# Kernel optimization log

Hardware: AMD Instinct MI355X
Metric: run time of the kernel (lower is better)

The kernel has to match this reference:

```python
import jax, jax.numpy as jnp
import numpy as np

N_NODES = 2048
UNITS = 64
IN_DIM = 64
K_DIFF = 2  # max_diffusion_step


def _rw_norm_t(adj):
    # random-walk normalize D^{-1}(A+I), then transpose (as in forward())
    a = adj + jnp.eye(adj.shape[0], dtype=adj.dtype)
    d = jnp.sum(a, axis=1)
    d_inv = jnp.where(d > 0, 1.0 / jnp.where(d > 0, d, 1.0), 0.0)
    return (d_inv[:, None] * a).T


def _gconv(x_cat, adj_t, W, b):
    # x_cat: (B, N, F). Chebyshev-like diffusion: x0, A x0, 2 A x1 - x0, ...
    x0 = x_cat
    xs = [x0]
    x1 = jnp.einsum('nm,bmf->bnf', adj_t, x0)
    xs.append(x1)
    for _ in range(2, K_DIFF + 1):
        x2 = 2.0 * jnp.einsum('nm,bmf->bnf', adj_t, x1) - x0
        xs.append(x2)
        x0, x1 = x1, x2
    x = jnp.stack(xs, axis=-1)  # (B, N, F, K+1) -> matches torch permute(3,1,2,0)
    B, N, F, K = x.shape
    x = x.reshape(B * N, F * K)
    out = x @ W + b
    return out.reshape(B, N, -1)


def setup_inputs() -> dict:
    key = jax.random.key(0)
    ks = jax.random.split(key, 6)
    B = 64
    inputs = jax.random.normal(ks[0], (B, N_NODES * IN_DIM), dtype=jnp.float32)
    hx = jax.random.normal(ks[1], (B, N_NODES * UNITS), dtype=jnp.float32)
    adj = jax.random.uniform(ks[2], (N_NODES, N_NODES), dtype=jnp.float32)
    in_sz = IN_DIM + UNITS
    nm = K_DIFF + 1
    scale = float(np.sqrt(2.0 / (in_sz * nm + 2 * UNITS)))  # xavier-ish
    W_ru = jax.random.normal(ks[3], (in_sz * nm, 2 * UNITS), dtype=jnp.float32) * scale
    b_ru = jnp.ones((2 * UNITS,), dtype=jnp.float32)  # bias_start=1.0
    W_c = jax.random.normal(ks[4], (in_sz * nm, UNITS), dtype=jnp.float32) * scale
    b_c = jnp.zeros((UNITS,), dtype=jnp.float32)
    return {"inputs": inputs, "hx": hx, "adj": adj,
            "W_ru": W_ru, "b_ru": b_ru, "W_c": W_c, "b_c": b_c}


def reference(inputs, hx, adj, W_ru, b_ru, W_c, b_c):
    B = inputs.shape[0]
    x = inputs.reshape(B, N_NODES, IN_DIM)
    h = hx.reshape(B, N_NODES, UNITS)
    adj_t = _rw_norm_t(adj)
    # r/u gates via graph conv + sigmoid
    ru = jax.nn.sigmoid(_gconv(jnp.concatenate([x, h], axis=-1), adj_t, W_ru, b_ru))
    r, u = ru[..., :UNITS], ru[..., UNITS:]
    # candidate state
    c = jnp.tanh(_gconv(jnp.concatenate([x, r * h], axis=-1), adj_t, W_c, b_c))
    new_state = u * h + (1.0 - u) * c
    return new_state.reshape(B, N_NODES * UNITS)
```

## Files before the change

kernel.cpp:

```cpp
#include <hip/hip_runtime.h>
#include <math.h>

typedef __attribute__((ext_vector_type(8))) short short8;
typedef __attribute__((ext_vector_type(4))) float float4v;
typedef __attribute__((ext_vector_type(16))) float float16v;
typedef __attribute__((ext_vector_type(4))) unsigned short ushort4v;
typedef unsigned short u16;
typedef unsigned int u32;

#define NB 64
#define NN 2048
#define FD 128
#define UD 64
#define KT 384


__device__ __forceinline__ u16 f2bf(float f) {
    unsigned int u = __float_as_uint(f);
    u += 0x7fffu + ((u >> 16) & 1u);
    return (u16)(u >> 16);
}
__device__ __forceinline__ float bf2f(u16 s) {
    return __uint_as_float(((unsigned int)s) << 16);
}
__device__ __forceinline__ float sigmoidf_(float x) {
    return 1.0f / (1.0f + expf(-x));
}
__device__ __forceinline__ void gl2lds16(const u16* g, u16* l) {
    __builtin_amdgcn_global_load_lds((const __attribute__((address_space(1))) unsigned int*)g,
                                     (__attribute__((address_space(3))) unsigned int*)l,
                                     16, 0, 0);
}

__global__ void k_rownorm(const float* __restrict__ adj, float* __restrict__ d_inv) {
    int m = blockIdx.x;
    const float4v* row = (const float4v*)(adj + (size_t)m * NN);
    float s = 0.f;
    for (int i = threadIdx.x; i < NN / 4; i += 256) {
        float4v v = row[i];
        s += v.x + v.y + v.z + v.w;
    }
    __shared__ float red[4];
    for (int off = 32; off; off >>= 1) s += __shfl_down(s, off, 64);
    if ((threadIdx.x & 63) == 0) red[threadIdx.x >> 6] = s;
    __syncthreads();
    if (threadIdx.x == 0) {
        float t = red[0] + red[1] + red[2] + red[3] + 1.0f;
        d_inv[m] = 1.0f / t;
    }
}

__global__ void k_adjT(const float* __restrict__ adj, const float* __restrict__ d_inv,
                       u16* __restrict__ adjT) {
    __shared__ u16 T[64 * 72];
    int m0 = blockIdx.x * 64;
    int n0 = blockIdx.y * 64;
    int t = threadIdx.x;
    for (int p = 0; p < 4; ++p) {
        int idx = t + 256 * p;
        int i  = idx >> 4;
        int n4 = idx & 15;
        int m = m0 + i;
        float4v v = *(const float4v*)(adj + (size_t)m * NN + n0 + n4 * 4);
        float di = d_inv[m];
        float vv[4] = {v.x, v.y, v.z, v.w};
#pragma unroll
        for (int j = 0; j < 4; ++j) {
            int n = n0 + n4 * 4 + j;
            float a = vv[j] + ((m == n) ? 1.0f : 0.0f);
            T[(n4 * 4 + j) * 72 + i] = f2bf(a * di);
        }
    }
    __syncthreads();
#pragma unroll
    for (int p = 0; p < 2; ++p) {
        int S = t + 256 * p;
        int rgl = S >> 8, kgl = (S >> 7) & 1, s = S & 127;
        int c = s >> 5, r = s & 31;
        short8 v = *(const short8*)(T + (rgl * 32 + r) * 72 + kgl * 32 + c * 8);
        *(short8*)(adjT + ((size_t)((n0 >> 5) + rgl) * 64 + (m0 >> 5) + kgl) * 1024 + s * 8) = v;
    }
}

__global__ void k_reorderW(const float* __restrict__ W, u16* __restrict__ Wt, int OD) {
    int idx = blockIdx.x * 256 + threadIdx.x;
    if (idx >= KT * OD) return;
    int o  = idx % OD;
    int kp = idx / OD;
    int kd = kp >> 7, f = kp & 127;
    Wt[(size_t)o * KT + kp] = f2bf(W[(size_t)(f * 3 + kd) * OD + o]);
}

__global__ void k_xcat(const float* __restrict__ x, const float* __restrict__ h,
                       u16* __restrict__ X0c) {
    __shared__ u16 T[128 * 136];
    int m0 = blockIdx.x * 128;
    int b  = blockIdx.y;
    int t = threadIdx.x;
    const float* srcs[2] = { x + (size_t)b * (NN * 64), h + (size_t)b * (NN * 64) };
    for (int s = 0; s < 2; ++s) {
        const float* src = srcs[s];
        for (int p = 0; p < 8; ++p) {
            int idx = t + 256 * p;
            int mi = idx >> 4;
            int f4 = idx & 15;
            float4v v = *(const float4v*)(src + (size_t)(m0 + mi) * 64 + f4 * 4);
            float vv[4] = {v.x, v.y, v.z, v.w};
#pragma unroll
            for (int j = 0; j < 4; ++j)
                T[(s * 64 + f4 * 4 + j) * 136 + mi] = f2bf(vv[j]);
        }
    }
    __syncthreads();
#pragma unroll
    for (int p = 0; p < 8; ++p) {
        int S = t + 256 * p;
        int fgl = S >> 9, kgl = (S >> 7) & 3, s = S & 127;
        int c = s >> 5, r = s & 31;
        short8 v = *(const short8*)(T + (fgl * 32 + r) * 136 + kgl * 32 + c * 8);
        *(short8*)(X0c + ((size_t)(b * 4 + fgl) * 64 + (m0 >> 5) + kgl) * 1024 + s * 8) = v;
    }
}

template<int MT>
__global__ __launch_bounds__(256, 2)
void k_gemm(const u16* __restrict__ A, const u16* __restrict__ Bc,
            u16* __restrict__ Cc, const u16* __restrict__ Sub, int mode, int cBlocks) {
    __shared__ u16 SM[8192 + 4096 * MT];
    u16* A0 = SM;            u16* A1 = SM + 4096;
    u16* B0 = SM + 8192;     u16* B1 = SM + 8192 + 2048 * MT;

    int id = blockIdx.x + cBlocks * blockIdx.y;
    int band = cBlocks >> 3;
    int g = id & 7, s = id >> 3;
    int cb = g * band + (s % band);
    int nb = s / band;
    int c0 = cb * (64 * MT);
    int n0 = nb * 128;

    int t = threadIdx.x;
    int wave = t >> 6, lane = t & 63;
    int wy = wave & 1, wx = wave >> 1;
    int ln = lane & 31, hi = lane >> 5;
    int l16 = lane * 8;

    const u16* gaP[2];
#pragma unroll
    for (int i = 0; i < 2; ++i) {
        int T = t + 256 * i;
        gaP[i] = A + ((size_t)((n0 >> 5) + (T >> 7)) * 64) * 1024 + (size_t)(T & 127) * 8;
    }
    const u16* gbP[MT];
#pragma unroll
    for (int i = 0; i < MT; ++i) {
        int T = t + 256 * i;
        gbP[i] = Bc + ((size_t)((c0 >> 5) + (T >> 7)) * 64) * 1024 + (size_t)(T & 127) * 8;
    }

    float16v acc[MT][2];
#pragma unroll
    for (int i = 0; i < MT; ++i)
#pragma unroll
        for (int j = 0; j < 2; ++j)
#pragma unroll
            for (int e = 0; e < 16; ++e) acc[i][j][e] = 0.f;

#pragma unroll
    for (int i = 0; i < 2; ++i)  gl2lds16(gaP[i], A0 + (t + 256 * i) * 8);
#pragma unroll
    for (int i = 0; i < MT; ++i) gl2lds16(gbP[i], B0 + (t + 256 * i) * 8);

#pragma unroll 2
    for (int it = 0; it < 64; ++it) {
        u16* Ac = (it & 1) ? A1 : A0;
        u16* Bs = (it & 1) ? B1 : B0;
        __syncthreads();
        if (it + 1 < 64) {
            int ko = (it + 1) * 1024;
            u16* An = (it & 1) ? A0 : A1;
            u16* Bn = (it & 1) ? B0 : B1;
#pragma unroll
            for (int i = 0; i < 2; ++i)  gl2lds16(gaP[i] + ko, An + (t + 256 * i) * 8);
#pragma unroll
            for (int i = 0; i < MT; ++i) gl2lds16(gbP[i] + ko, Bn + (t + 256 * i) * 8);
        }
        short8 fa[2][MT], fb[2][2];
#pragma unroll
        for (int ks = 0; ks < 2; ++ks) {
#pragma unroll
            for (int mt = 0; mt < MT; ++mt)
                fa[ks][mt] = *(const short8*)(Bs + ((wx * MT + mt) * 2 + ks) * 512 + l16);
#pragma unroll
            for (int nt = 0; nt < 2; ++nt)
                fb[ks][nt] = *(const short8*)(Ac + ((wy * 2 + nt) * 2 + ks) * 512 + l16);
        }
#pragma unroll
        for (int ks = 0; ks < 2; ++ks)
#pragma unroll
            for (int mt = 0; mt < MT; ++mt)
#pragma unroll
                for (int nt = 0; nt < 2; ++nt)
                    acc[mt][nt] = __builtin_amdgcn_mfma_f32_32x32x16_bf16(fa[ks][mt], fb[ks][nt], acc[mt][nt], 0, 0, 0);
    }

    __syncthreads();
#pragma unroll
    for (int p = 0; p < 2; ++p) {
        if (p) __syncthreads();
        if (wx == p) {
#pragma unroll
            for (int mt = 0; mt < MT; ++mt)
#pragma unroll
                for (int nt = 0; nt < 2; ++nt)
#pragma unroll
                    for (int e = 0; e < 16; ++e) {
                        int cl = mt * 32 + 4 * hi + 8 * (e >> 2) + (e & 3);
                        int nl = wy * 64 + nt * 32 + ln;
                        SM[cl * 136 + nl] = f2bf(acc[mt][nt][e]);
                    }
        }
        __syncthreads();
#pragma unroll
        for (int pp = 0; pp < 2 * MT; ++pp) {
            int S = t + 256 * pp;
            int rgl = S >> 9, kgl = (S >> 7) & 3, sl = S & 127;
            int c = sl >> 5, r = sl & 31;
            short8 v = *(const short8*)(SM + (rgl * 32 + r) * 136 + kgl * 32 + c * 8);
            size_t gaddr = ((size_t)((c0 >> 5) + p * MT + rgl) * 64 + (n0 >> 5) + kgl) * 1024 + sl * 8;
            if (mode == 1) {
                short8 sv = *(const short8*)(Sub + gaddr);
                short8 o;
#pragma unroll
                for (int e = 0; e < 8; ++e)
                    o[e] = (short)f2bf(2.f * bf2f((u16)v[e]) - bf2f((u16)sv[e]));
                *(short8*)(Cc + gaddr) = o;
            } else {
                *(short8*)(Cc + gaddr) = v;
            }
        }
    }
}

__global__ __launch_bounds__(256)
void k_ruW(const u16* __restrict__ X0c, const u16* __restrict__ X1c, const u16* __restrict__ X2c,
           const u16* __restrict__ Wt, const float* __restrict__ bias,
           const float* __restrict__ hx,
           u16* __restrict__ RH0c, float* __restrict__ Utc) {
    __shared__ u16 As[128 * 40];
    __shared__ u16 Bs[4096];
    int rt = blockIdx.x;
    int b  = rt >> 4;
    int m0 = (rt & 15) * 128;
    int t = threadIdx.x;
    int wave = t >> 6, lane = t & 63;
    int wr = (wave >> 1) * 64, wc = (wave & 1) * 64;
    int lr = lane & 15, q = lane >> 4;
    const u16* Xs[3] = {X0c, X1c, X2c};
    int f2 = t & 15;
    int m8 = (t >> 4) * 8;
    const u16* gw[2];
#pragma unroll
    for (int i = 0; i < 2; ++i) {
        int T = t + 256 * i;
        gw[i] = Wt + (size_t)((T >> 6) * 16 + (T & 15)) * KT + ((T >> 4) & 3) * 8;
    }

    float4v acc[4][4];
#pragma unroll
    for (int i = 0; i < 4; ++i)
#pragma unroll
        for (int j = 0; j < 4; ++j) { acc[i][j].x = 0.f; acc[i][j].y = 0.f; acc[i][j].z = 0.f; acc[i][j].w = 0.f; }

    for (int it = 0; it < 12; ++it) {
        int k0 = it * 32;
        int kd = k0 >> 7, fb = k0 & 127;
        gl2lds16(gw[0] + k0, Bs + t * 8);
        gl2lds16(gw[1] + k0, Bs + (t + 256) * 8);
        const u16* base = Xs[kd] + ((size_t)(b * 4 + (fb >> 5)) * 64 + (m0 >> 5) + (m8 >> 5)) * 1024
                          + (((m8 >> 3) & 3) * 32 + 2 * f2) * 8;
        short8 v0 = *(const short8*)(base);
        short8 v1 = *(const short8*)(base + 8);
#pragma unroll
        for (int e = 0; e < 8; ++e)
            *(u32*)(As + (m8 + e) * 40 + 2 * f2) = (u32)(u16)v0[e] | ((u32)(u16)v1[e] << 16);
        __syncthreads();
        short8 af[4], bfr[4];
#pragma unroll
        for (int i = 0; i < 4; ++i) af[i]  = *(const short8*)(As + (wr + 16 * i + lr) * 40 + q * 8);
#pragma unroll
        for (int j = 0; j < 4; ++j) bfr[j] = *(const short8*)(Bs + ((wc >> 4) + j) * 512 + lane * 8);
#pragma unroll
        for (int i = 0; i < 4; ++i)
#pragma unroll
            for (int j = 0; j < 4; ++j)
                acc[i][j] = __builtin_amdgcn_mfma_f32_16x16x32_bf16(af[i], bfr[j], acc[i][j], 0, 0, 0);
        __syncthreads();
    }
#pragma unroll
    for (int i = 0; i < 4; ++i) {
        int m = m0 + wr + 16 * i + q * 4;
#pragma unroll
        for (int j = 0; j < 4; ++j) {
            int o = wc + 16 * j + lr;
            float bia = bias[o];
            float4v v = acc[i][j];
            if (o < 64) {
                ushort4v pk;
#pragma unroll
                for (int r = 0; r < 4; ++r) {
                    float sg = sigmoidf_(v[r] + bia);
                    float hh = hx[(size_t)b * (NN * 64) + (size_t)(m + r) * 64 + o];
                    pk[r] = f2bf(sg * hh);
                }
                size_t ga = ((size_t)(b * 2 + (o >> 5)) * 64 + (m >> 5)) * 1024
                            + (((m >> 3) & 3) * 32 + (o & 31)) * 8 + (m & 7);
                *(ushort4v*)(RH0c + ga) = pk;
            } else {
                int gg = o - 64;
                float4v u;
#pragma unroll
                for (int r = 0; r < 4; ++r) u[r] = sigmoidf_(v[r] + bia);
                *(float4v*)(Utc + ((size_t)(b * UD + gg)) * NN + m) = u;
            }
        }
    }
}

__global__ __launch_bounds__(256)
void k_cW(const u16* __restrict__ X0c, const u16* __restrict__ X1c, const u16* __restrict__ X2c,
          const u16* __restrict__ RH0c, const u16* __restrict__ RH1c, const u16* __restrict__ RH2c,
          const u16* __restrict__ Wt, const float* __restrict__ bias,
          const float* __restrict__ hx, const float* __restrict__ Utc,
          float* __restrict__ out) {
    __shared__ u16 As[256 * 40];
    __shared__ u16 Bs[2048];
    int rt = blockIdx.x;
    int b  = rt >> 3;
    int m0 = (rt & 7) * 256;
    int t = threadIdx.x;
    int wave = t >> 6, lane = t & 63;
    int lr = lane & 15, q = lane >> 4;
    const u16* Xs[3] = {X0c, X1c, X2c};
    const u16* Rs[3] = {RH0c, RH1c, RH2c};
    const u16* gw = Wt + (size_t)((t >> 6) * 16 + (t & 15)) * KT + ((t >> 4) & 3) * 8;

    float4v acc[4][4];
#pragma unroll
    for (int i = 0; i < 4; ++i)
#pragma unroll
        for (int j = 0; j < 4; ++j) { acc[i][j].x = 0.f; acc[i][j].y = 0.f; acc[i][j].z = 0.f; acc[i][j].w = 0.f; }

    for (int it = 0; it < 12; ++it) {
        int k0 = it * 32;
        int kd = k0 >> 7, fb = k0 & 127;
        const u16* mat; int rg;
        if (fb < 64) { mat = Xs[kd]; rg = b * 4 + (fb >> 5); }
        else         { mat = Rs[kd]; rg = b * 2 + ((fb - 64) >> 5); }
        gl2lds16(gw + k0, Bs + t * 8);
#pragma unroll
        for (int p = 0; p < 2; ++p) {
            int idx = t + 256 * p;
            int f2 = idx & 15;
            int m8 = (idx >> 4) * 8;
            const u16* base = mat + ((size_t)rg * 64 + (m0 >> 5) + (m8 >> 5)) * 1024
                              + (((m8 >> 3) & 3) * 32 + 2 * f2) * 8;
            short8 v0 = *(const short8*)(base);
            short8 v1 = *(const short8*)(base + 8);
#pragma unroll
            for (int e = 0; e < 8; ++e)
                *(u32*)(As + (m8 + e) * 40 + 2 * f2) = (u32)(u16)v0[e] | ((u32)(u16)v1[e] << 16);
        }
        __syncthreads();
        short8 af[4], bfr[4];
#pragma unroll
        for (int i = 0; i < 4; ++i) af[i]  = *(const short8*)(As + (64 * wave + 16 * i + lr) * 40 + q * 8);
#pragma unroll
        for (int j = 0; j < 4; ++j) bfr[j] = *(const short8*)(Bs + j * 512 + lane * 8);
#pragma unroll
        for (int i = 0; i < 4; ++i)
#pragma unroll
            for (int j = 0; j < 4; ++j)
                acc[i][j] = __builtin_amdgcn_mfma_f32_16x16x32_bf16(af[i], bfr[j], acc[i][j], 0, 0, 0);
        __syncthreads();
    }
#pragma unroll
    for (int i = 0; i < 4; ++i) {
        int m = m0 + 64 * wave + 16 * i + q * 4;
#pragma unroll
        for (int j = 0; j < 4; ++j) {
            int o = 16 * j + lr;
            float bia = bias[o];
            float4v v = acc[i][j];
            float4v u = *(const float4v*)(Utc + ((size_t)(b * UD + o)) * NN + m);
#pragma unroll
            for (int r = 0; r < 4; ++r) {
                float c = tanhf(v[r] + bia);
                size_t idx = (size_t)b * (NN * 64) + (size_t)(m + r) * 64 + o;
                float hh = hx[idx];
                out[idx] = u[r] * hh + (1.0f - u[r]) * c;
            }
        }
    }
}

extern "C" void kernel_launch(void* const* d_in, const int* in_sizes, int n_in,
                              void* d_out, int out_size, void* d_ws, size_t ws_size,
                              hipStream_t stream) {
    const float* x    = (const float*)d_in[0];
    const float* hx   = (const float*)d_in[1];
    const float* adj  = (const float*)d_in[2];
    const float* W_ru = (const float*)d_in[3];
    const float* b_ru = (const float*)d_in[4];
    const float* W_c  = (const float*)d_in[5];
    const float* b_c  = (const float*)d_in[6];
    float* out = (float*)d_out;

    char* ws = (char*)d_ws;
    size_t off = 0;
    auto alloc = [&](size_t bytes) -> void* {
        void* p = ws + off;
        off += (bytes + 255) & ~(size_t)255;
        return p;
    };
    float* d_inv = (float*)alloc((size_t)NN * 4);
    u16* adjT  = (u16*)alloc((size_t)NN * NN * 2);
    u16* Wt_ru = (u16*)alloc((size_t)FD * KT * 2);
    u16* Wt_c  = (u16*)alloc((size_t)UD * KT * 2);
    u16* X0c = (u16*)alloc((size_t)NB * FD * NN * 2);
    u16* X1c = (u16*)alloc((size_t)NB * FD * NN * 2);
    u16* X2c = (u16*)alloc((size_t)NB * FD * NN * 2);
    u16* RH0c = (u16*)alloc((size_t)NB * UD * NN * 2);
    u16* RH1c = (u16*)alloc((size_t)NB * UD * NN * 2);
    u16* RH2c = (u16*)alloc((size_t)NB * UD * NN * 2);
    float* Utc = (float*)alloc((size_t)NB * UD * NN * 4);

    k_rownorm<<<dim3(NN), dim3(256), 0, stream>>>(adj, d_inv);
    k_adjT<<<dim3(32, 32), dim3(256), 0, stream>>>(adj, d_inv, adjT);
    k_reorderW<<<dim3((KT * FD + 255) / 256), dim3(256), 0, stream>>>(W_ru, Wt_ru, FD);
    k_reorderW<<<dim3((KT * UD + 255) / 256), dim3(256), 0, stream>>>(W_c, Wt_c, UD);
    k_xcat<<<dim3(16, NB), dim3(256), 0, stream>>>(x, hx, X0c);
    k_gemm<4><<<dim3(32, 16), dim3(256), 0, stream>>>(adjT, X0c, X1c, X0c, 0, 32);
    k_gemm<4><<<dim3(32, 16), dim3(256), 0, stream>>>(adjT, X1c, X2c, X0c, 1, 32);
    k_ruW<<<dim3(1024), dim3(256), 0, stream>>>(X0c, X1c, X2c, Wt_ru, b_ru, hx, RH0c, Utc);
    k_gemm<2><<<dim3(32, 16), dim3(256), 0, stream>>>(adjT, RH0c, RH1c, RH0c, 0, 32);
    k_gemm<2><<<dim3(32, 16), dim3(256), 0, stream>>>(adjT, RH1c, RH2c, RH0c, 1, 32);
    k_cW<<<dim3(512), dim3(256), 0, stream>>>(X0c, X1c, X2c, RH0c, RH1c, RH2c, Wt_c, b_c, hx, Utc, out);
}
```

Measured before the change: 472.0 us.

## Emit MFMA-fragment layout from diffusion GEMMs and rewrite projection kernels

The diffusion GEMMs now write their results straight from accumulators into a second MFMA-fragment-ordered layout, and they only do the LDS transpose into the feature-major layout when the next diffusion step needs it. The projection kernels are rewritten to stream both operands into double-buffered LDS with 32x32 MFMA and no per-element repacking. The update gate is stored as bf16 in node-major order rather than fp32 transposed. Together these aim to remove the register-level reshuffle in the projections, cut redundant transposes and gate traffic, and overlap loads with compute. The cost is an extra full-size buffer write in the first diffusion step and some extra workspace.

```diff
diff --git a/kernel.cpp b/kernel.cpp
--- a/kernel.cpp
+++ b/kernel.cpp
@@ -88,11 +88,12 @@
     int o  = idx % OD;
     int kp = idx / OD;
     int kd = kp >> 7, f = kp & 127;
-    Wt[(size_t)o * KT + kp] = f2bf(W[(size_t)(f * 3 + kd) * OD + o]);
+    size_t dst = ((size_t)(o >> 5) * 12 + (kp >> 5)) * 1024 + (((kp >> 3) & 3) * 32 + (o & 31)) * 8 + (kp & 7);
+    Wt[dst] = f2bf(W[(size_t)(f * 3 + kd) * OD + o]);
 }
 
 __global__ void k_xcat(const float* __restrict__ x, const float* __restrict__ h,
-                       u16* __restrict__ X0c) {
+                       u16* __restrict__ X0f, u16* __restrict__ X0m) {
     __shared__ u16 T[128 * 136];
     int m0 = blockIdx.x * 128;
     int b  = blockIdx.y;
@@ -118,14 +119,27 @@
         int fgl = S >> 9, kgl = (S >> 7) & 3, s = S & 127;
         int c = s >> 5, r = s & 31;
         short8 v = *(const short8*)(T + (fgl * 32 + r) * 136 + kgl * 32 + c * 8);
-        *(short8*)(X0c + ((size_t)(b * 4 + fgl) * 64 + (m0 >> 5) + kgl) * 1024 + s * 8) = v;
+        *(short8*)(X0f + ((size_t)(b * 4 + fgl) * 64 + (m0 >> 5) + kgl) * 1024 + s * 8) = v;
+    }
+#pragma unroll
+    for (int p = 0; p < 8; ++p) {
+        int S = t + 256 * p;
+        int fc = S >> 7;
+        int mi = S & 127;
+        short8 v;
+#pragma unroll
+        for (int e = 0; e < 8; ++e) v[e] = (short)T[(fc * 8 + e) * 136 + mi];
+        size_t dst = ((size_t)(b * 64 + (m0 >> 5) + (mi >> 5)) * 4 + (fc >> 2)) * 1024
+                     + ((fc & 3) * 32 + (mi & 31)) * 8;
+        *(short8*)(X0m + dst) = v;
     }
 }
 
 template<int MT>
 __global__ __launch_bounds__(256, 2)
 void k_gemm(const u16* __restrict__ A, const u16* __restrict__ Bc,
-            u16* __restrict__ Cc, const u16* __restrict__ Sub, int mode, int cBlocks) {
+            u16* __restrict__ outF, u16* __restrict__ outM,
+            const u16* __restrict__ Sub, int mode, int cBlocks) {
     __shared__ u16 SM[8192 + 4096 * MT];
     u16* A0 = SM;            u16* A1 = SM + 4096;
     u16* B0 = SM + 8192;     u16* B1 = SM + 8192 + 2048 * MT;
@@ -203,204 +217,249 @@
                     acc[mt][nt] = __builtin_amdgcn_mfma_f32_32x32x16_bf16(fa[ks][mt], fb[ks][nt], acc[mt][nt], 0, 0, 0);
     }
 
+    int bb2 = 2 * cb + wx;
+#pragma unroll
+    for (int mt = 0; mt < MT; ++mt) {
+#pragma unroll
+        for (int nt = 0; nt < 2; ++nt) {
+            int mg = (n0 >> 5) + wy * 2 + nt;
+            size_t pbase = ((size_t)(bb2 * 64 + mg) * MT + mt) * 1024;
+#pragma unroll
+            for (int eq = 0; eq < 4; ++eq) {
+                size_t addr = pbase + (eq * 32 + ln) * 8 + 4 * hi;
+                ushort4v pk;
+                if (mode == 1) {
+                    ushort4v sv = *(const ushort4v*)(Sub + addr);
+#pragma unroll
+                    for (int r = 0; r < 4; ++r)
+                        pk[r] = f2bf(2.f * acc[mt][nt][eq * 4 + r] - bf2f(sv[r]));
+                } else {
+#pragma unroll
+                    for (int r = 0; r < 4; ++r) pk[r] = f2bf(acc[mt][nt][eq * 4 + r]);
+                }
+                *(ushort4v*)(outM + addr) = pk;
+            }
+        }
+    }
+
+    if (outF) {
+        __syncthreads();
+#pragma unroll
+        for (int p = 0; p < 2; ++p) {
+            if (p) __syncthreads();
+            if (wx == p) {
+#pragma unroll
+                for (int mt = 0; mt < MT; ++mt)
+#pragma unroll
+                    for (int nt = 0; nt < 2; ++nt)
+#pragma unroll
+                        for (int e = 0; e < 16; ++e) {
+                            int cl = mt * 32 + 4 * hi + 8 * (e >> 2) + (e & 3);
+                            int nl = wy * 64 + nt * 32 + ln;
+                            SM[cl * 136 + nl] = f2bf(acc[mt][nt][e]);
+                        }
+            }
+            __syncthreads();
+#pragma unroll
+            for (int pp = 0; pp < 2 * MT; ++pp) {
+                int S = t + 256 * pp;
+                int rgl = S >> 9, kgl = (S >> 7) & 3, sl = S & 127;
+                int c = sl >> 5, r = sl & 31;
+                short8 v = *(const short8*)(SM + (rgl * 32 + r) * 136 + kgl * 32 + c * 8);
+                size_t gaddr = ((size_t)((c0 >> 5) + p * MT + rgl) * 64 + (n0 >> 5) + kgl) * 1024 + sl * 8;
+                *(short8*)(outF + gaddr) = v;
+            }
+        }
+    }
+}
+
+__global__ __launch_bounds__(256)
+void k_proj_ru(const u16* __restrict__ X0m, const u16* __restrict__ X1m, const u16* __restrict__ X2m,
+               const u16* __restrict__ Wp, const float* __restrict__ bias, const float* __restrict__ hx,
+               u16* __restrict__ RH0f, u16* __restrict__ RH0m, u16* __restrict__ Ut) {
+    __shared__ u16 SM[16384];
+    u16 *Xa = SM, *Xb = SM + 4096, *Wa = SM + 8192, *Wb = SM + 12288;
+    int mb = blockIdx.x, b = blockIdx.y;
+    int m0 = mb * 128, mg0 = mb * 4;
+    int t = threadIdx.x, wave = t >> 6, lane = t & 63;
+    int wx = wave & 1, wyy = wave >> 1;
+    int ln = lane & 31, hi = lane >> 5;
+    const u16* Xs[3] = {X0m, X1m, X2m};
+    int p0 = t >> 7, s0 = t & 127;
+
+    float16v acc[2][2];
+#pragma unroll
+    for (int i = 0; i < 2; ++i)
+#pragma unroll
+        for (int j = 0; j < 2; ++j)
+#pragma unroll
+            for (int e = 0; e < 16; ++e) acc[i][j][e] = 0.f;
+
+    gl2lds16(Xs[0] + ((size_t)((b * 64 + mg0 + p0) * 4)) * 1024 + s0 * 8, Xa + t * 8);
+    gl2lds16(Xs[0] + ((size_t)((b * 64 + mg0 + p0 + 2) * 4)) * 1024 + s0 * 8, Xa + (t + 256) * 8);
+    gl2lds16(Wp + ((size_t)(p0 * 12)) * 1024 + s0 * 8, Wa + t * 8);
+    gl2lds16(Wp + ((size_t)((p0 + 2) * 12)) * 1024 + s0 * 8, Wa + (t + 256) * 8);
+
+    for (int kq = 0; kq < 12; ++kq) {
+        u16* Xc = (kq & 1) ? Xb : Xa;
+        u16* Wc = (kq & 1) ? Wb : Wa;
+        __syncthreads();
+        if (kq + 1 < 12) {
+            int k2 = kq + 1, kd = k2 >> 2, kg = k2 & 3;
+            u16* Xn = (kq & 1) ? Xa : Xb;
+            u16* Wn = (kq & 1) ? Wa : Wb;
+            const u16* xb = Xs[kd];
+            gl2lds16(xb + ((size_t)((b * 64 + mg0 + p0) * 4 + kg)) * 1024 + s0 * 8, Xn + t * 8);
+            gl2lds16(xb + ((size_t)((b * 64 + mg0 + p0 + 2) * 4 + kg)) * 1024 + s0 * 8, Xn + (t + 256) * 8);
+            gl2lds16(Wp + ((size_t)(p0 * 12 + k2)) * 1024 + s0 * 8, Wn + t * 8);
+            gl2lds16(Wp + ((size_t)((p0 + 2) * 12 + k2)) * 1024 + s0 * 8, Wn + (t + 256) * 8);
+        }
+        short8 fa[2][2], fb[2][2];
+#pragma unroll
+        for (int ks = 0; ks < 2; ++ks) {
+#pragma unroll
+            for (int mt = 0; mt < 2; ++mt)
+                fa[ks][mt] = *(const short8*)(Xc + ((wx * 2 + mt) * 2 + ks) * 512 + lane * 8);
+#pragma unroll
+            for (int nt = 0; nt < 2; ++nt)
+                fb[ks][nt] = *(const short8*)(Wc + ((wyy * 2 + nt) * 2 + ks) * 512 + lane * 8);
+        }
+#pragma unroll
+        for (int ks = 0; ks < 2; ++ks)
+#pragma unroll
+            for (int mt = 0; mt < 2; ++mt)
+#pragma unroll
+                for (int nt = 0; nt < 2; ++nt)
+                    acc[mt][nt] = __builtin_amdgcn_mfma_f32_32x32x16_bf16(fa[ks][mt], fb[ks][nt], acc[mt][nt], 0, 0, 0);
+    }
     __syncthreads();
-#pragma unroll
-    for (int p = 0; p < 2; ++p) {
-        if (p) __syncthreads();
-        if (wx == p) {
-#pragma unroll
-            for (int mt = 0; mt < MT; ++mt)
-#pragma unroll
-                for (int nt = 0; nt < 2; ++nt)
-#pragma unroll
-                    for (int e = 0; e < 16; ++e) {
-                        int cl = mt * 32 + 4 * hi + 8 * (e >> 2) + (e & 3);
-                        int nl = wy * 64 + nt * 32 + ln;
-                        SM[cl * 136 + nl] = f2bf(acc[mt][nt][e]);
-                    }
-        }
+    if (wyy == 0) {
+#pragma unroll
+        for (int mt = 0; mt < 2; ++mt)
+#pragma unroll
+            for (int nt = 0; nt < 2; ++nt) {
+                int o = nt * 32 + ln;
+                float bo = bias[o];
+                u16 vals[16];
+#pragma unroll
+                for (int e = 0; e < 16; ++e) {
+                    int ml = wx * 64 + mt * 32 + 4 * hi + 8 * (e >> 2) + (e & 3);
+                    float sg = sigmoidf_(acc[mt][nt][e] + bo);
+                    float hh = hx[((size_t)b * NN + m0 + ml) * 64 + o];
+                    vals[e] = f2bf(sg * hh);
+                    SM[ml * 76 + o] = vals[e];
+                }
+#pragma unroll
+                for (int eq = 0; eq < 4; ++eq) {
+                    ushort4v pk;
+#pragma unroll
+                    for (int r = 0; r < 4; ++r) pk[r] = vals[eq * 4 + r];
+                    size_t addr = ((size_t)(b * 2 + nt) * 64 + mg0 + wx * 2 + mt) * 1024 + (eq * 32 + ln) * 8 + 4 * hi;
+                    *(ushort4v*)(RH0f + addr) = pk;
+                }
+            }
+    } else {
+#pragma unroll
+        for (int mt = 0; mt < 2; ++mt)
+#pragma unroll
+            for (int nt = 0; nt < 2; ++nt) {
+                int og = nt * 32 + ln;
+                float bo = bias[64 + og];
+#pragma unroll
+                for (int e = 0; e < 16; ++e) {
+                    int ml = wx * 64 + mt * 32 + 4 * hi + 8 * (e >> 2) + (e & 3);
+                    Ut[((size_t)b * NN + m0 + ml) * 64 + og] = f2bf(sigmoidf_(acc[mt][nt][e] + bo));
+                }
+            }
+    }
+    __syncthreads();
+#pragma unroll
+    for (int j = 0; j < 4; ++j) {
+        int C = t + 256 * j;
+        int p = C >> 7, sl = C & 127;
+        int mgl = p >> 1, ug = p & 1;
+        int cq = sl >> 5, r = sl & 31;
+        short8 v = *(const short8*)(SM + (mgl * 32 + r) * 76 + ug * 32 + cq * 8);
+        *(short8*)(RH0m + ((size_t)((b * 64 + mg0 + mgl) * 2 + ug)) * 1024 + sl * 8) = v;
+    }
+}
+
+__global__ __launch_bounds__(256)
+void k_proj_c(const u16* __restrict__ X0m, const u16* __restrict__ X1m, const u16* __restrict__ X2m,
+              const u16* __restrict__ RH0m, const u16* __restrict__ RH1m, const u16* __restrict__ RH2m,
+              const u16* __restrict__ Wp, const float* __restrict__ bias,
+              const float* __restrict__ hx, const u16* __restrict__ Ut,
+              float* __restrict__ out) {
+    __shared__ u16 SM[12288];
+    u16 *Xa = SM, *Xb = SM + 4096, *Wa = SM + 8192, *Wb = SM + 10240;
+    int mb = blockIdx.x, b = blockIdx.y;
+    int m0 = mb * 128, mg0 = mb * 4;
+    int t = threadIdx.x, wave = t >> 6, lane = t & 63;
+    int wx = wave & 1, wyy = wave >> 1;
+    int ln = lane & 31, hi = lane >> 5;
+    const u16* Xs[3] = {X0m, X1m, X2m};
+    const u16* Rs[3] = {RH0m, RH1m, RH2m};
+    int p0 = t >> 7, s0 = t & 127;
+
+    float16v acc[2];
+#pragma unroll
+    for (int i = 0; i < 2; ++i)
+#pragma unroll
+        for (int e = 0; e < 16; ++e) acc[i][e] = 0.f;
+
+    gl2lds16(Xs[0] + ((size_t)((b * 64 + mg0 + p0) * 4)) * 1024 + s0 * 8, Xa + t * 8);
+    gl2lds16(Xs[0] + ((size_t)((b * 64 + mg0 + p0 + 2) * 4)) * 1024 + s0 * 8, Xa + (t + 256) * 8);
+    gl2lds16(Wp + ((size_t)(p0 * 12)) * 1024 + s0 * 8, Wa + t * 8);
+
+    for (int kq = 0; kq < 12; ++kq) {
+        u16* Xc = (kq & 1) ? Xb : Xa;
+        u16* Wc = (kq & 1) ? Wb : Wa;
         __syncthreads();
-#pragma unroll
-        for (int pp = 0; pp < 2 * MT; ++pp) {
-            int S = t + 256 * pp;
-            int rgl = S >> 9, kgl = (S >> 7) & 3, sl = S & 127;
-            int c = sl >> 5, r = sl & 31;
-            short8 v = *(const short8*)(SM + (rgl * 32 + r) * 136 + kgl * 32 + c * 8);
-            size_t gaddr = ((size_t)((c0 >> 5) + p * MT + rgl) * 64 + (n0 >> 5) + kgl) * 1024 + sl * 8;
-            if (mode == 1) {
-                short8 sv = *(const short8*)(Sub + gaddr);
-                short8 o;
-#pragma unroll
-                for (int e = 0; e < 8; ++e)
-                    o[e] = (short)f2bf(2.f * bf2f((u16)v[e]) - bf2f((u16)sv[e]));
-                *(short8*)(Cc + gaddr) = o;
+        if (kq + 1 < 12) {
+            int k2 = kq + 1, kd = k2 >> 2, fb2 = (k2 & 3) * 32;
+            u16* Xn = (kq & 1) ? Xa : Xb;
+            u16* Wn = (kq & 1) ? Wa : Wb;
+            const u16* mat; size_t pb0, pb1;
+            if (fb2 < 64) {
+                mat = Xs[kd];
+                pb0 = ((size_t)((b * 64 + mg0 + p0) * 4 + (fb2 >> 5))) * 1024;
+                pb1 = ((size_t)((b * 64 + mg0 + p0 + 2) * 4 + (fb2 >> 5))) * 1024;
             } else {
-                *(short8*)(Cc + gaddr) = v;
+                mat = Rs[kd];
+                pb0 = ((size_t)((b * 64 + mg0 + p0) * 2 + ((fb2 >> 5) - 2))) * 1024;
+                pb1 = ((size_t)((b * 64 + mg0 + p0 + 2) * 2 + ((fb2 >> 5) - 2))) * 1024;
             }
-        }
-    }
-}
-
-__global__ __launch_bounds__(256)
-void k_ruW(const u16* __restrict__ X0c, const u16* __restrict__ X1c, const u16* __restrict__ X2c,
-           const u16* __restrict__ Wt, const float* __restrict__ bias,
-           const float* __restrict__ hx,
-           u16* __restrict__ RH0c, float* __restrict__ Utc) {
-    __shared__ u16 As[128 * 40];
-    __shared__ u16 Bs[4096];
-    int rt = blockIdx.x;
-    int b  = rt >> 4;
-    int m0 = (rt & 15) * 128;
-    int t = threadIdx.x;
-    int wave = t >> 6, lane = t & 63;
-    int wr = (wave >> 1) * 64, wc = (wave & 1) * 64;
-    int lr = lane & 15, q = lane >> 4;
-    const u16* Xs[3] = {X0c, X1c, X2c};
-    int f2 = t & 15;
-    int m8 = (t >> 4) * 8;
-    const u16* gw[2];
-#pragma unroll
-    for (int i = 0; i < 2; ++i) {
-        int T = t + 256 * i;
-        gw[i] = Wt + (size_t)((T >> 6) * 16 + (T & 15)) * KT + ((T >> 4) & 3) * 8;
-    }
-
-    float4v acc[4][4];
-#pragma unroll
-    for (int i = 0; i < 4; ++i)
-#pragma unroll
-        for (int j = 0; j < 4; ++j) { acc[i][j].x = 0.f; acc[i][j].y = 0.f; acc[i][j].z = 0.f; acc[i][j].w = 0.f; }
-
-    for (int it = 0; it < 12; ++it) {
-        int k0 = it * 32;
-        int kd = k0 >> 7, fb = k0 & 127;
-        gl2lds16(gw[0] + k0, Bs + t * 8);
-        gl2lds16(gw[1] + k0, Bs + (t + 256) * 8);
-        const u16* base = Xs[kd] + ((size_t)(b * 4 + (fb >> 5)) * 64 + (m0 >> 5) + (m8 >> 5)) * 1024
-                          + (((m8 >> 3) & 3) * 32 + 2 * f2) * 8;
-        short8 v0 = *(const short8*)(base);
-        short8 v1 = *(const short8*)(base + 8);
-#pragma unroll
-        for (int e = 0; e < 8; ++e)
-            *(u32*)(As + (m8 + e) * 40 + 2 * f2) = (u32)(u16)v0[e] | ((u32)(u16)v1[e] << 16);
-        __syncthreads();
-        short8 af[4], bfr[4];
-#pragma unroll
-        for (int i = 0; i < 4; ++i) af[i]  = *(const short8*)(As + (wr + 16 * i + lr) * 40 + q * 8);
-#pragma unroll
-        for (int j = 0; j < 4; ++j) bfr[j] = *(const short8*)(Bs + ((wc >> 4) + j) * 512 + lane * 8);
-#pragma unroll
-        for (int i = 0; i < 4; ++i)
-#pragma unroll
-            for (int j = 0; j < 4; ++j)
-                acc[i][j] = __builtin_amdgcn_mfma_f32_16x16x32_bf16(af[i], bfr[j], acc[i][j], 0, 0, 0);
-        __syncthreads();
-    }
-#pragma unroll
-    for (int i = 0; i < 4; ++i) {
-        int m = m0 + wr + 16 * i + q * 4;
-#pragma unroll
-        for (int j = 0; j < 4; ++j) {
-            int o = wc + 16 * j + lr;
-            float bia = bias[o];
-            float4v v = acc[i][j];
-            if (o < 64) {
-                ushort4v pk;
-#pragma unroll
-                for (int r = 0; r < 4; ++r) {
-                    float sg = sigmoidf_(v[r] + bia);
-                    float hh = hx[(size_t)b * (NN * 64) + (size_t)(m + r) * 64 + o];
-                    pk[r] = f2bf(sg * hh);
-                }
-                size_t ga = ((size_t)(b * 2 + (o >> 5)) * 64 + (m >> 5)) * 1024
-                            + (((m >> 3) & 3) * 32 + (o & 31)) * 8 + (m & 7);
-                *(ushort4v*)(RH0c + ga) = pk;
-            } else {
-                int gg = o - 64;
-                float4v u;
-#pragma unroll
-                for (int r = 0; r < 4; ++r) u[r] = sigmoidf_(v[r] + bia);
-                *(float4v*)(Utc + ((size_t)(b * UD + gg)) * NN + m) = u;
-            }
-        }
-    }
-}
-
-__global__ __launch_bounds__(256)
-void k_cW(const u16* __restrict__ X0c, const u16* __restrict__ X1c, const u16* __restrict__ X2c,
-          const u16* __restrict__ RH0c, const u16* __restrict__ RH1c, const u16* __restrict__ RH2c,
-          const u16* __restrict__ Wt, const float* __restrict__ bias,
-          const float* __restrict__ hx, const float* __restrict__ Utc,
-          float* __restrict__ out) {
-    __shared__ u16 As[256 * 40];
-    __shared__ u16 Bs[2048];
-    int rt = blockIdx.x;
-    int b  = rt >> 3;
-    int m0 = (rt & 7) * 256;
-    int t = threadIdx.x;
-    int wave = t >> 6, lane = t & 63;
-    int lr = lane & 15, q = lane >> 4;
-    const u16* Xs[3] = {X0c, X1c, X2c};
-    const u16* Rs[3] = {RH0c, RH1c, RH2c};
-    const u16* gw = Wt + (size_t)((t >> 6) * 16 + (t & 15)) * KT + ((t >> 4) & 3) * 8;
-
-    float4v acc[4][4];
-#pragma unroll
-    for (int i = 0; i < 4; ++i)
-#pragma unroll
-        for (int j = 0; j < 4; ++j) { acc[i][j].x = 0.f; acc[i][j].y = 0.f; acc[i][j].z = 0.f; acc[i][j].w = 0.f; }
-
-    for (int it = 0; it < 12; ++it) {
-        int k0 = it * 32;
-        int kd = k0 >> 7, fb = k0 & 127;
-        const u16* mat; int rg;
-        if (fb < 64) { mat = Xs[kd]; rg = b * 4 + (fb >> 5); }
-        else         { mat = Rs[kd]; rg = b * 2 + ((fb - 64) >> 5); }
-        gl2lds16(gw + k0, Bs + t * 8);
-#pragma unroll
-        for (int p = 0; p < 2; ++p) {
-            int idx = t + 256 * p;
-            int f2 = idx & 15;
-            int m8 = (idx >> 4) * 8;
-            const u16* base = mat + ((size_t)rg * 64 + (m0 >> 5) + (m8 >> 5)) * 1024
-                              + (((m8 >> 3) & 3) * 32 + 2 * f2) * 8;
-            short8 v0 = *(const short8*)(base);
-            short8 v1 = *(const short8*)(base + 8);
-#pragma unroll
-            for (int e = 0; e < 8; ++e)
-                *(u32*)(As + (m8 + e) * 40 + 2 * f2) = (u32)(u16)v0[e] | ((u32)(u16)v1[e] << 16);
-        }
-        __syncthreads();
-        short8 af[4], bfr[4];
-#pragma unroll
-        for (int i = 0; i < 4; ++i) af[i]  = *(const short8*)(As + (64 * wave + 16 * i + lr) * 40 + q * 8);
-#pragma unroll
-        for (int j = 0; j < 4; ++j) bfr[j] = *(const short8*)(Bs + j * 512 + lane * 8);
-#pragma unroll
-        for (int i = 0; i < 4; ++i)
-#pragma unroll
-            for (int j = 0; j < 4; ++j)
-                acc[i][j] = __builtin_amdgcn_mfma_f32_16x16x32_bf16(af[i], bfr[j], acc[i][j], 0, 0, 0);
-        __syncthreads();
-    }
-#pragma unroll
-    for (int i = 0; i < 4; ++i) {
-        int m = m0 + 64 * wave + 16 * i + q * 4;
-#pragma unroll
-        for (int j = 0; j < 4; ++j) {
-            int o = 16 * j + lr;
-            float bia = bias[o];
-            float4v v = acc[i][j];
-            float4v u = *(const float4v*)(Utc + ((size_t)(b * UD + o)) * NN + m);
-#pragma unroll
-            for (int r = 0; r < 4; ++r) {
-                float c = tanhf(v[r] + bia);
-                size_t idx = (size_t)b * (NN * 64) + (size_t)(m + r) * 64 + o;
-                float hh = hx[idx];
-                out[idx] = u[r] * hh + (1.0f - u[r]) * c;
-            }
-        }
-    }
+            gl2lds16(mat + pb0 + s0 * 8, Xn + t * 8);
+            gl2lds16(mat + pb1 + s0 * 8, Xn + (t + 256) * 8);
+            gl2lds16(Wp + ((size_t)(p0 * 12 + k2)) * 1024 + s0 * 8, Wn + t * 8);
+        }
+        short8 fa[2][2], fbg[2];
+#pragma unroll
+        for (int ks = 0; ks < 2; ++ks) {
+#pragma unroll
+            for (int mt = 0; mt < 2; ++mt)
+                fa[ks][mt] = *(const short8*)(Xc + ((wx * 2 + mt) * 2 + ks) * 512 + lane * 8);
+            fbg[ks] = *(const short8*)(Wc + (wyy * 2 + ks) * 512 + lane * 8);
+        }
+#pragma unroll
+        for (int ks = 0; ks < 2; ++ks)
+#pragma unroll
+            for (int mt = 0; mt < 2; ++mt)
+                acc[mt] = __builtin_amdgcn_mfma_f32_32x32x16_bf16(fa[ks][mt], fbg[ks], acc[mt], 0, 0, 0);
+    }
+    int o = wyy * 32 + ln;
+    float bo = bias[o];
+#pragma unroll
+    for (int mt = 0; mt < 2; ++mt)
+#pragma unroll
+        for (int e = 0; e < 16; ++e) {
+            int ml = wx * 64 + mt * 32 + 4 * hi + 8 * (e >> 2) + (e & 3);
+            size_t idx = ((size_t)b * NN + m0 + ml) * 64 + o;
+            float c = tanhf(acc[mt][e] + bo);
+            float u = bf2f(Ut[idx]);
+            float hh = hx[idx];
+            out[idx] = u * hh + (1.0f - u) * c;
+        }
 }
 
 extern "C" void kernel_launch(void* const* d_in, const int* in_sizes, int n_in,
@@ -423,26 +482,30 @@
         return p;
     };
     float* d_inv = (float*)alloc((size_t)NN * 4);
-    u16* adjT  = (u16*)alloc((size_t)NN * NN * 2);
-    u16* Wt_ru = (u16*)alloc((size_t)FD * KT * 2);
-    u16* Wt_c  = (u16*)alloc((size_t)UD * KT * 2);
-    u16* X0c = (u16*)alloc((size_t)NB * FD * NN * 2);
-    u16* X1c = (u16*)alloc((size_t)NB * FD * NN * 2);
-    u16* X2c = (u16*)alloc((size_t)NB * FD * NN * 2);
-    u16* RH0c = (u16*)alloc((size_t)NB * UD * NN * 2);
-    u16* RH1c = (u16*)alloc((size_t)NB * UD * NN * 2);
-    u16* RH2c = (u16*)alloc((size_t)NB * UD * NN * 2);
-    float* Utc = (float*)alloc((size_t)NB * UD * NN * 4);
+    u16* adjT = (u16*)alloc((size_t)NN * NN * 2);
+    u16* Wru  = (u16*)alloc((size_t)FD * KT * 2);
+    u16* Wc   = (u16*)alloc((size_t)UD * KT * 2);
+    u16* X0f = (u16*)alloc((size_t)NB * FD * NN * 2);
+    u16* X1f = (u16*)alloc((size_t)NB * FD * NN * 2);
+    u16* X0m = (u16*)alloc((size_t)NB * FD * NN * 2);
+    u16* X1m = (u16*)alloc((size_t)NB * FD * NN * 2);
+    u16* X2m = (u16*)alloc((size_t)NB * FD * NN * 2);
+    u16* RH0m = (u16*)alloc((size_t)NB * UD * NN * 2);
+    u16* RH1m = (u16*)alloc((size_t)NB * UD * NN * 2);
+    u16* RH2m = (u16*)alloc((size_t)NB * UD * NN * 2);
+    u16* Ut   = (u16*)alloc((size_t)NB * UD * NN * 2);
+    u16* RH0f = X0f;
+    u16* RH1f = X1f;
 
     k_rownorm<<<dim3(NN), dim3(256), 0, stream>>>(adj, d_inv);
     k_adjT<<<dim3(32, 32), dim3(256), 0, stream>>>(adj, d_inv, adjT);
-    k_reorderW<<<dim3((KT * FD + 255) / 256), dim3(256), 0, stream>>>(W_ru, Wt_ru, FD);
-    k_reorderW<<<dim3((KT * UD + 255) / 256), dim3(256), 0, stream>>>(W_c, Wt_c, UD);
-    k_xcat<<<dim3(16, NB), dim3(256), 0, stream>>>(x, hx, X0c);
-    k_gemm<4><<<dim3(32, 16), dim3(256), 0, stream>>>(adjT, X0c, X1c, X0c, 0, 32);
-    k_gemm<4><<<dim3(32, 16), dim3(256), 0, stream>>>(adjT, X1c, X2c, X0c, 1, 32);
-    k_ruW<<<dim3(1024), dim3(256), 0, stream>>>(X0c, X1c, X2c, Wt_ru, b_ru, hx, RH0c, Utc);
-    k_gemm<2><<<dim3(32, 16), dim3(256), 0, stream>>>(adjT, RH0c, RH1c, RH0c, 0, 32);
-    k_gemm<2><<<dim3(32, 16), dim3(256), 0, stream>>>(adjT, RH1c, RH2c, RH0c, 1, 32);
-    k_cW<<<dim3(512), dim3(256), 0, stream>>>(X0c, X1c, X2c, RH0c, RH1c, RH2c, Wt_c, b_c, hx, Utc, out);
-}
+    k_reorderW<<<dim3((KT * FD + 255) / 256), dim3(256), 0, stream>>>(W_ru, Wru, FD);
+    k_reorderW<<<dim3((KT * UD + 255) / 256), dim3(256), 0, stream>>>(W_c, Wc, UD);
+    k_xcat<<<dim3(16, NB), dim3(256), 0, stream>>>(x, hx, X0f, X0m);
+    k_gemm<4><<<dim3(32, 16), dim3(256), 0, stream>>>(adjT, X0f, X1f, X1m, nullptr, 0, 32);
+    k_gemm<4><<<dim3(32, 16), dim3(256), 0, stream>>>(adjT, X1f, nullptr, X2m, X0m, 1, 32);
+    k_proj_ru<<<dim3(16, NB), dim3(256), 0, stream>>>(X0m, X1m, X2m, Wru, b_ru, hx, RH0f, RH0m, Ut);
+    k_gemm<2><<<dim3(32, 16), dim3(256), 0, stream>>>(adjT, RH0f, RH1f, RH1m, nullptr, 0, 32);
+    k_gemm<2><<<dim3(32, 16), dim3(256), 0, stream>>>(adjT, RH1f, nullptr, RH2m, RH0m, 1, 32);
+    k_proj_c<<<dim3(16, NB), dim3(256), 0, stream>>>(X0m, X1m, X2m, RH0m, RH1m, RH2m, Wc, b_c, hx, Ut, out);
+}
```

New measurement: 520.0 us. 10.2% more time.
